# Kernel optimization log

Hardware: AMD Instinct MI355X
Metric: run time of the kernel (lower is better)

Reference implementation:

```python
import jax, jax.numpy as jnp
import numpy as np

N_NODES = 100000
N_EDGES = 1250000
D = 64


def _sage_conv(x, src, dst, W_l, b_l, W_r, n_nodes):
    # message = x[src]; scatter-mean onto dst; then lin_l(mean) + lin_r(x)
    msg = x[src]                                               # [E, D]
    agg = jax.ops.segment_sum(msg, dst, num_segments=n_nodes)  # [N, D]
    cnt = jax.ops.segment_sum(jnp.ones((src.shape[0],), x.dtype), dst,
                              num_segments=n_nodes)            # [N]
    mean = agg / jnp.maximum(cnt, 1.0)[:, None]
    return mean @ W_l + b_l + x @ W_r


def setup_inputs() -> dict:
    key = jax.random.key(0)
    ks = jax.random.split(key, 8)
    s = 1.0 / np.sqrt(D)
    x = jax.random.normal(ks[0], (N_NODES, D), dtype=jnp.float32)
    edge_index = jax.random.randint(ks[1], (2, N_EDGES), 0, N_NODES, dtype=jnp.int32)
    W_l1 = jax.random.normal(ks[2], (D, D), dtype=jnp.float32) * s
    b_l1 = jnp.zeros((D,), jnp.float32)
    W_r1 = jax.random.normal(ks[3], (D, D), dtype=jnp.float32) * s
    W_l2 = jax.random.normal(ks[4], (D, D), dtype=jnp.float32) * s
    b_l2 = jnp.zeros((D,), jnp.float32)
    W_r2 = jax.random.normal(ks[5], (D, D), dtype=jnp.float32) * s
    return {"x": x, "edge_index": edge_index,
            "W_l1": W_l1, "b_l1": b_l1, "W_r1": W_r1,
            "W_l2": W_l2, "b_l2": b_l2, "W_r2": W_r2}


def reference(x, edge_index, W_l1, b_l1, W_r1, W_l2, b_l2, W_r2):
    src, dst = edge_index[0], edge_index[1]
    n = x.shape[0]
    h = jax.nn.relu(_sage_conv(x, src, dst, W_l1, b_l1, W_r1, n))
    return _sage_conv(h, src, dst, W_l2, b_l2, W_r2, n)
```

## Files before the change

### kernel.cpp

```cpp
#include <hip/hip_runtime.h>

#define N_NODES 100000
#define N_EDGES 1250000
#define D 64
#define ZERO_NODE N_NODES

#define BIN_SHIFT 8
#define BIN_NODES 256
#define NBINS ((N_NODES + BIN_NODES - 1) >> BIN_SHIFT)
#define BIN_CAP 3712
#define BIN_SLAB (BIN_CAP + 3 * BIN_NODES)
#define CHUNK 2048
#define NCHUNK ((N_EDGES + CHUNK - 1) / CHUNK)
#define CCAP 32
#define CONV4 (N_NODES * D / 4)

#define SLAB_INTS (NBINS * BIN_SLAB)

typedef __attribute__((ext_vector_type(8))) short short8;
typedef __attribute__((ext_vector_type(4))) float f32x4;

__device__ inline unsigned short f2bf(float f) {
    unsigned int u = __float_as_uint(f);
    unsigned int r = (u + 0x7fffu + ((u >> 16) & 1u)) >> 16;
    return (unsigned short)r;
}
__device__ inline void acc_bf4(float4& c, uint2 u) {
    c.x += __uint_as_float(u.x << 16);
    c.y += __uint_as_float(u.x & 0xffff0000u);
    c.z += __uint_as_float(u.y << 16);
    c.w += __uint_as_float(u.y & 0xffff0000u);
}

__global__ __launch_bounds__(1024)
void part_convert_kernel(const float4* __restrict__ xin, ushort4* __restrict__ xb,
                         unsigned int* __restrict__ xb_zrow,
                         unsigned int* __restrict__ h_zrow,
                         const float* __restrict__ Wl1, const float* __restrict__ Wr1,
                         const float* __restrict__ Wl2, const float* __restrict__ Wr2,
                         unsigned short* __restrict__ wt,
                         const int* __restrict__ src, const int* __restrict__ dst,
                         int* __restrict__ cslab, unsigned short* __restrict__ ccnt) {
    __shared__ int lcur[NBINS];

    const int t = threadIdx.x;
    const int c = blockIdx.x;
    if (t < NBINS) lcur[t] = 0;

    const int g0 = c * 1024 + t;
    const int gsz = NCHUNK * 1024;
    for (int g = g0; g < CONV4; g += gsz) {
        float4 v = xin[g];
        ushort4 u;
        u.x = f2bf(v.x); u.y = f2bf(v.y); u.z = f2bf(v.z); u.w = f2bf(v.w);
        xb[g] = u;
    }
    if (g0 < 32) { xb_zrow[g0] = 0u; h_zrow[g0] = 0u; }
    if (g0 < 2 * 64 * 128) {
        int layer = g0 >> 13;
        int n = (g0 >> 7) & 63;
        int k = g0 & 127;
        const float* W = layer ? (k < 64 ? Wl2 : Wr2) : (k < 64 ? Wl1 : Wr1);
        wt[g0] = f2bf(W[(k & 63) * D + n]);
    }
    __syncthreads();

    const int e0 = c * CHUNK;
    int cnt = N_EDGES - e0; if (cnt > CHUNK) cnt = CHUNK;
    for (int i = t; i < cnt; i += 1024) {
        int d = dst[e0 + i];
        int s = src[e0 + i];
        int b = d >> BIN_SHIFT;
        int r = atomicAdd(&lcur[b], 1);
        if (r < CCAP)
            cslab[(c * NBINS + b) * CCAP + r] = (s << BIN_SHIFT) | (d & (BIN_NODES - 1));
    }
    __syncthreads();

    if (t < NBINS) {
        int v = lcur[t];
        ccnt[t * NCHUNK + c] = (unsigned short)(v < CCAP ? v : CCAP);
    }
}

__global__ __launch_bounds__(1024)
void build_kernel(const int* __restrict__ cslab, const unsigned short* __restrict__ ccnt,
                  int* __restrict__ deg_out, int* __restrict__ rstart_out,
                  int* __restrict__ slabs) {
    __shared__ int soff[NCHUNK];
    __shared__ int scnt[NCHUNK];
    __shared__ int stage[BIN_CAP];
    __shared__ int hist[BIN_NODES];
    __shared__ int cur[BIN_NODES];
    __shared__ int wsum[16];
    __shared__ int wsum2[16];
    __shared__ int tot_s;

    const int b = blockIdx.x;
    const int t = threadIdx.x;
    const int lane = t & 63, wave = t >> 6;
    const int nb0 = b << BIN_SHIFT;

    int v = (t < NCHUNK) ? (int)ccnt[b * NCHUNK + t] : 0;
    int sv = v;
    for (int off = 1; off < 64; off <<= 1) {
        int u = __shfl_up(sv, off);
        if (lane >= off) sv += u;
    }
    if (lane == 63) wsum[wave] = sv;
    if (t < BIN_NODES) hist[t] = 0;
    __syncthreads();
    int wpre = 0;
    for (int w = 0; w < wave; ++w) wpre += wsum[w];
    int excl = sv + wpre - v;
    if (t < NCHUNK) { soff[t] = excl; scnt[t] = v; }
    if (t == NCHUNK - 1) tot_s = excl + v;
    __syncthreads();

    int cntb = tot_s; if (cntb > BIN_CAP) cntb = BIN_CAP;

    if (t < NCHUNK) {
        int base = soff[t], n = scnt[t];
        const int* p = &cslab[(t * NBINS + b) * CCAP];
        for (int r = 0; r < n; ++r) {
            int pos = base + r;
            if (pos < BIN_CAP) stage[pos] = p[r];
        }
    }
    __syncthreads();

    for (int i = t; i < cntb; i += 1024)
        atomicAdd(&hist[stage[i] & (BIN_NODES - 1)], 1);
    __syncthreads();

    int h = (t < BIN_NODES) ? hist[t] : 0;
    int p = (h + 3) & ~3;
    int s2 = p;
    for (int off = 1; off < 64; off <<= 1) {
        int u = __shfl_up(s2, off);
        if (lane >= off) s2 += u;
    }
    if (lane == 63) wsum2[wave] = s2;
    __syncthreads();
    int wpre2 = 0;
    for (int w = 0; w < wave; ++w) wpre2 += wsum2[w];
    if (t < BIN_NODES) {
        int excl2 = s2 + wpre2 - p;
        int rs = b * BIN_SLAB + excl2;
        cur[t] = rs;
        int n = nb0 + t;
        if (n < N_NODES) {
            deg_out[n] = h;
            rstart_out[n] = rs;
            for (int j = h; j < p; ++j) slabs[rs + j] = ZERO_NODE;
        }
    }
    __syncthreads();

    for (int i = t; i < cntb; i += 1024) {
        int pk = stage[i];
        int pos = atomicAdd(&cur[pk & (BIN_NODES - 1)], 1);
        slabs[pos] = pk >> BIN_SHIFT;
    }
}

template <typename TOUT>
__global__ __launch_bounds__(256, 6)
void fused_layer_kernel(const unsigned short* __restrict__ xin,
                        const int* __restrict__ rstart,
                        const int* __restrict__ deg,
                        const int* __restrict__ sorted_src,
                        const unsigned short* __restrict__ wt,
                        const float* __restrict__ bl,
                        TOUT* __restrict__ out,
                        int relu) {
    __shared__ __align__(16) unsigned short sA[32][136];

    const uint2* __restrict__ xin64 = (const uint2*)xin;

    const int tid = threadIdx.x;
    const int row0 = blockIdx.x * 32;

    const int wave = tid >> 6;
    const int lane = tid & 63;
    const int q  = lane >> 4;
    const int f2 = lane & 15;

#pragma unroll
    for (int j = 0; j < 2; ++j) {
        const int rb = wave * 8 + 4 * j;
        const int n0 = row0 + rb, n1 = n0 + 1, n2 = n0 + 2, n3 = n0 + 3;

        int dg0 = deg[n0], dg1 = deg[n1], dg2 = deg[n2], dg3 = deg[n3];
        int st0 = rstart[n0], st1 = rstart[n1], st2 = rstart[n2], st3 = rstart[n3];
        int pd0 = (dg0 + 3) & ~3, pd1 = (dg1 + 3) & ~3;
        int pd2 = (dg2 + 3) & ~3, pd3 = (dg3 + 3) & ~3;
        int m0 = pd0 > 64 ? 64 : pd0, m1 = pd1 > 64 ? 64 : pd1;
        int m2 = pd2 > 64 ? 64 : pd2, m3 = pd3 > 64 ? 64 : pd3;

        int idx0 = ZERO_NODE, idx1 = ZERO_NODE, idx2 = ZERO_NODE, idx3 = ZERO_NODE;
        if (lane < m0) idx0 = sorted_src[st0 + lane];
        if (lane < m1) idx1 = sorted_src[st1 + lane];
        if (lane < m2) idx2 = sorted_src[st2 + lane];
        if (lane < m3) idx3 = sorted_src[st3 + lane];
        uint2 xr0 = xin64[(size_t)n0 * 16 + f2];
        uint2 xr1 = xin64[(size_t)n1 * 16 + f2];
        uint2 xr2 = xin64[(size_t)n2 * 16 + f2];
        uint2 xr3 = xin64[(size_t)n3 * 16 + f2];

        float4 c0 = make_float4(0.f, 0.f, 0.f, 0.f);
        float4 c1 = make_float4(0.f, 0.f, 0.f, 0.f);
        float4 c2 = make_float4(0.f, 0.f, 0.f, 0.f);
        float4 c3 = make_float4(0.f, 0.f, 0.f, 0.f);

        int q0 = m0 >> 2, q1 = m1 >> 2, q2 = m2 >> 2, q3 = m3 >> 2;
        int qa = q0 > q1 ? q0 : q1, qb = q2 > q3 ? q2 : q3;
        int quads = qa > qb ? qa : qb;
        int t = 0;
        for (; t + 2 <= quads; t += 2) {
            int e00 = __shfl(idx0, 4 * t + q), e01 = __shfl(idx0, 4 * t + 4 + q);
            int e10 = __shfl(idx1, 4 * t + q), e11 = __shfl(idx1, 4 * t + 4 + q);
            int e20 = __shfl(idx2, 4 * t + q), e21 = __shfl(idx2, 4 * t + 4 + q);
            int e30 = __shfl(idx3, 4 * t + q), e31 = __shfl(idx3, 4 * t + 4 + q);
            uint2 u00 = xin64[(size_t)e00 * 16 + f2];
            uint2 u01 = xin64[(size_t)e01 * 16 + f2];
            uint2 u10 = xin64[(size_t)e10 * 16 + f2];
            uint2 u11 = xin64[(size_t)e11 * 16 + f2];
            uint2 u20 = xin64[(size_t)e20 * 16 + f2];
            uint2 u21 = xin64[(size_t)e21 * 16 + f2];
            uint2 u30 = xin64[(size_t)e30 * 16 + f2];
            uint2 u31 = xin64[(size_t)e31 * 16 + f2];
            acc_bf4(c0, u00); acc_bf4(c0, u01);
            acc_bf4(c1, u10); acc_bf4(c1, u11);
            acc_bf4(c2, u20); acc_bf4(c2, u21);
            acc_bf4(c3, u30); acc_bf4(c3, u31);
        }
        for (; t < quads; ++t) {
            int e00 = __shfl(idx0, 4 * t + q);
            int e10 = __shfl(idx1, 4 * t + q);
            int e20 = __shfl(idx2, 4 * t + q);
            int e30 = __shfl(idx3, 4 * t + q);
            uint2 u00 = xin64[(size_t)e00 * 16 + f2];
            uint2 u10 = xin64[(size_t)e10 * 16 + f2];
            uint2 u20 = xin64[(size_t)e20 * 16 + f2];
            uint2 u30 = xin64[(size_t)e30 * 16 + f2];
            acc_bf4(c0, u00); acc_bf4(c1, u10);
            acc_bf4(c2, u20); acc_bf4(c3, u30);
        }

        if (__builtin_expect(pd0 > 64, 0)) {
            for (int base = 64; base < pd0; base += 64) {
                int m = pd0 - base; if (m > 64) m = 64;
                int idx = ZERO_NODE;
                if (lane < m) idx = sorted_src[st0 + base + lane];
                int qds = m >> 2;
                for (int tt = 0; tt < qds; ++tt) {
                    int e = __shfl(idx, 4 * tt + q);
                    acc_bf4(c0, xin64[(size_t)e * 16 + f2]);
                }
            }
        }
        if (__builtin_expect(pd1 > 64, 0)) {
            for (int base = 64; base < pd1; base += 64) {
                int m = pd1 - base; if (m > 64) m = 64;
                int idx = ZERO_NODE;
                if (lane < m) idx = sorted_src[st1 + base + lane];
                int qds = m >> 2;
                for (int tt = 0; tt < qds; ++tt) {
                    int e = __shfl(idx, 4 * tt + q);
                    acc_bf4(c1, xin64[(size_t)e * 16 + f2]);
                }
            }
        }
        if (__builtin_expect(pd2 > 64, 0)) {
            for (int base = 64; base < pd2; base += 64) {
                int m = pd2 - base; if (m > 64) m = 64;
                int idx = ZERO_NODE;
                if (lane < m) idx = sorted_src[st2 + base + lane];
                int qds = m >> 2;
                for (int tt = 0; tt < qds; ++tt) {
                    int e = __shfl(idx, 4 * tt + q);
                    acc_bf4(c2, xin64[(size_t)e * 16 + f2]);
                }
            }
        }
        if (__builtin_expect(pd3 > 64, 0)) {
            for (int base = 64; base < pd3; base += 64) {
                int m = pd3 - base; if (m > 64) m = 64;
                int idx = ZERO_NODE;
                if (lane < m) idx = sorted_src[st3 + base + lane];
                int qds = m >> 2;
                for (int tt = 0; tt < qds; ++tt) {
                    int e = __shfl(idx, 4 * tt + q);
                    acc_bf4(c3, xin64[(size_t)e * 16 + f2]);
                }
            }
        }

        c0.x += __shfl_xor(c0.x, 16); c0.y += __shfl_xor(c0.y, 16);
        c0.z += __shfl_xor(c0.z, 16); c0.w += __shfl_xor(c0.w, 16);
        c1.x += __shfl_xor(c1.x, 16); c1.y += __shfl_xor(c1.y, 16);
        c1.z += __shfl_xor(c1.z, 16); c1.w += __shfl_xor(c1.w, 16);
        c2.x += __shfl_xor(c2.x, 16); c2.y += __shfl_xor(c2.y, 16);
        c2.z += __shfl_xor(c2.z, 16); c2.w += __shfl_xor(c2.w, 16);
        c3.x += __shfl_xor(c3.x, 16); c3.y += __shfl_xor(c3.y, 16);
        c3.z += __shfl_xor(c3.z, 16); c3.w += __shfl_xor(c3.w, 16);
        c0.x += __shfl_xor(c0.x, 32); c0.y += __shfl_xor(c0.y, 32);
        c0.z += __shfl_xor(c0.z, 32); c0.w += __shfl_xor(c0.w, 32);
        c1.x += __shfl_xor(c1.x, 32); c1.y += __shfl_xor(c1.y, 32);
        c1.z += __shfl_xor(c1.z, 32); c1.w += __shfl_xor(c1.w, 32);
        c2.x += __shfl_xor(c2.x, 32); c2.y += __shfl_xor(c2.y, 32);
        c2.z += __shfl_xor(c2.z, 32); c2.w += __shfl_xor(c2.w, 32);
        c3.x += __shfl_xor(c3.x, 32); c3.y += __shfl_xor(c3.y, 32);
        c3.z += __shfl_xor(c3.z, 32); c3.w += __shfl_xor(c3.w, 32);

        float i0 = 1.0f / (float)(dg0 > 0 ? dg0 : 1);
        float i1 = 1.0f / (float)(dg1 > 0 ? dg1 : 1);
        float i2 = 1.0f / (float)(dg2 > 0 ? dg2 : 1);
        float i3 = 1.0f / (float)(dg3 > 0 ? dg3 : 1);
        if (q == 0) {
            unsigned int p0, p1;
            p0 = (unsigned int)f2bf(c0.x * i0) | ((unsigned int)f2bf(c0.y * i0) << 16);
            p1 = (unsigned int)f2bf(c0.z * i0) | ((unsigned int)f2bf(c0.w * i0) << 16);
            *(uint2*)&sA[rb + 0][f2 * 4] = make_uint2(p0, p1);
            *(uint2*)&sA[rb + 0][64 + f2 * 4] = xr0;
            p0 = (unsigned int)f2bf(c1.x * i1) | ((unsigned int)f2bf(c1.y * i1) << 16);
            p1 = (unsigned int)f2bf(c1.z * i1) | ((unsigned int)f2bf(c1.w * i1) << 16);
            *(uint2*)&sA[rb + 1][f2 * 4] = make_uint2(p0, p1);
            *(uint2*)&sA[rb + 1][64 + f2 * 4] = xr1;
            p0 = (unsigned int)f2bf(c2.x * i2) | ((unsigned int)f2bf(c2.y * i2) << 16);
            p1 = (unsigned int)f2bf(c2.z * i2) | ((unsigned int)f2bf(c2.w * i2) << 16);
            *(uint2*)&sA[rb + 2][f2 * 4] = make_uint2(p0, p1);
            *(uint2*)&sA[rb + 2][64 + f2 * 4] = xr2;
            p0 = (unsigned int)f2bf(c3.x * i3) | ((unsigned int)f2bf(c3.y * i3) << 16);
            p1 = (unsigned int)f2bf(c3.z * i3) | ((unsigned int)f2bf(c3.w * i3) << 16);
            *(uint2*)&sA[rb + 3][f2 * 4] = make_uint2(p0, p1);
            *(uint2*)&sA[rb + 3][64 + f2 * 4] = xr3;
        }
    }
    __syncthreads();

    const int tm = wave & 1;
    const int tn0 = (wave >> 1) * 2;
    const int mrow = tm * 16 + (lane & 15);
    const int kq = (lane >> 4) * 8;

    short8 afr[4];
#pragma unroll
    for (int kk = 0; kk < 4; ++kk)
        afr[kk] = *(const short8*)&sA[mrow][kk * 32 + kq];

#pragma unroll
    for (int ti = 0; ti < 2; ++ti) {
        const int tn = tn0 + ti;
        const int col = tn * 16 + (lane & 15);
        float bias = bl[col];
        f32x4 acc = {bias, bias, bias, bias};
#pragma unroll
        for (int kk = 0; kk < 4; ++kk) {
            short8 bfr = *(const short8*)&wt[col * 128 + kk * 32 + kq];
            acc = __builtin_amdgcn_mfma_f32_16x16x32_bf16(afr[kk], bfr, acc, 0, 0, 0);
        }
        const int r0 = row0 + tm * 16 + (lane >> 4) * 4;
#pragma unroll
        for (int reg = 0; reg < 4; ++reg) {
            float o = relu ? fmaxf(acc[reg], 0.f) : acc[reg];
            if constexpr (__hip_internal::is_same<TOUT, unsigned short>::value)
                out[(size_t)(r0 + reg) * D + col] = f2bf(o);
            else
                out[(size_t)(r0 + reg) * D + col] = o;
        }
    }
}

extern "C" void kernel_launch(void* const* d_in, const int* in_sizes, int n_in,
                              void* d_out, int out_size, void* d_ws, size_t ws_size,
                              hipStream_t stream) {
    const float* x   = (const float*)d_in[0];
    const int*   ei  = (const int*)d_in[1];
    const float* Wl1 = (const float*)d_in[2];
    const float* b1  = (const float*)d_in[3];
    const float* Wr1 = (const float*)d_in[4];
    const float* Wl2 = (const float*)d_in[5];
    const float* b2  = (const float*)d_in[6];
    const float* Wr2 = (const float*)d_in[7];

    const int* src = ei;
    const int* dst = ei + N_EDGES;

    int* cslab = (int*)d_ws;
    unsigned short* ccnt = (unsigned short*)(cslab + NCHUNK * NBINS * CCAP);
    int* deg    = cslab + NCHUNK * NBINS * CCAP + 120000;
    int* rstart = deg + N_NODES;
    int* slabs  = rstart + N_NODES;
    unsigned short* wt_all = (unsigned short*)(slabs + SLAB_INTS);
    unsigned short* wt1 = wt_all;
    unsigned short* wt2 = wt_all + 64 * 128;
    unsigned short* h = wt_all + 2 * 64 * 128;
    float* out = (float*)d_out;
    unsigned short* xb = (unsigned short*)d_out;

    const int dense_blocks = N_NODES / 32;

    part_convert_kernel<<<NCHUNK, 1024, 0, stream>>>(
        (const float4*)x, (ushort4*)xb,
        (unsigned int*)(xb + (size_t)ZERO_NODE * D),
        (unsigned int*)(h + (size_t)ZERO_NODE * D),
        Wl1, Wr1, Wl2, Wr2, wt_all,
        src, dst, cslab, ccnt);

    build_kernel<<<NBINS, 1024, 0, stream>>>(cslab, ccnt, deg, rstart, slabs);

    fused_layer_kernel<unsigned short><<<dense_blocks, 256, 0, stream>>>(
        xb, rstart, deg, slabs, wt1, b1, h, 1);
    fused_layer_kernel<float><<<dense_blocks, 256, 0, stream>>>(
        h, rstart, deg, slabs, wt2, b2, out, 0);
}
```

Baseline: 201.8 us.

## Fold CSR build into layer kernels with per-block LDS edge bucketing

Removes the separate build kernel. The partition kernel now bins edges into 32-node bins per 4096-edge chunk, and each fused layer block gathers its bin's chunk lists into shared memory. There it histograms and scatters them to form its own padded neighbour lists before aggregation. This drops one launch and the global slab round-trip. In exchange, the bucketing work is repeated in both layers, every block reads a small count array and slab covering all chunks, and fixed caps (16 per chunk-bin, 704 per bin) can silently drop edges if exceeded.

```diff
diff --git a/kernel.cpp b/kernel.cpp
--- a/kernel.cpp
+++ b/kernel.cpp
@@ -5,17 +5,16 @@
 #define D 64
 #define ZERO_NODE N_NODES
 
-#define BIN_SHIFT 8
-#define BIN_NODES 256
-#define NBINS ((N_NODES + BIN_NODES - 1) >> BIN_SHIFT)
-#define BIN_CAP 3712
-#define BIN_SLAB (BIN_CAP + 3 * BIN_NODES)
-#define CHUNK 2048
-#define NCHUNK ((N_EDGES + CHUNK - 1) / CHUNK)
-#define CCAP 32
+#define BSHIFT 5
+#define BINSZ 32
+#define NBIN (N_NODES / BINSZ)
+#define CH 4096
+#define NC ((N_EDGES + CH - 1) / CH)
+#define CAP 16
 #define CONV4 (N_NODES * D / 4)
 
-#define SLAB_INTS (NBINS * BIN_SLAB)
+#define RAWCAP 704
+#define ELCAP 832
 
 typedef __attribute__((ext_vector_type(8))) short short8;
 typedef __attribute__((ext_vector_type(4))) float f32x4;
@@ -40,15 +39,15 @@
                          const float* __restrict__ Wl2, const float* __restrict__ Wr2,
                          unsigned short* __restrict__ wt,
                          const int* __restrict__ src, const int* __restrict__ dst,
-                         int* __restrict__ cslab, unsigned short* __restrict__ ccnt) {
-    __shared__ int lcur[NBINS];
+                         int* __restrict__ cslab, unsigned char* __restrict__ ccnt) {
+    __shared__ int lcur[NBIN];
 
     const int t = threadIdx.x;
     const int c = blockIdx.x;
-    if (t < NBINS) lcur[t] = 0;
+    for (int i = t; i < NBIN; i += 1024) lcur[i] = 0;
 
     const int g0 = c * 1024 + t;
-    const int gsz = NCHUNK * 1024;
+    const int gsz = NC * 1024;
     for (int g = g0; g < CONV4; g += gsz) {
         float4 v = xin[g];
         ushort4 u;
@@ -65,148 +64,123 @@
     }
     __syncthreads();
 
-    const int e0 = c * CHUNK;
-    int cnt = N_EDGES - e0; if (cnt > CHUNK) cnt = CHUNK;
+    const int e0 = c * CH;
+    int cnt = N_EDGES - e0; if (cnt > CH) cnt = CH;
     for (int i = t; i < cnt; i += 1024) {
         int d = dst[e0 + i];
         int s = src[e0 + i];
-        int b = d >> BIN_SHIFT;
+        int b = d >> BSHIFT;
         int r = atomicAdd(&lcur[b], 1);
-        if (r < CCAP)
-            cslab[(c * NBINS + b) * CCAP + r] = (s << BIN_SHIFT) | (d & (BIN_NODES - 1));
-    }
-    __syncthreads();
-
-    if (t < NBINS) {
-        int v = lcur[t];
-        ccnt[t * NCHUNK + c] = (unsigned short)(v < CCAP ? v : CCAP);
-    }
-}
-
-__global__ __launch_bounds__(1024)
-void build_kernel(const int* __restrict__ cslab, const unsigned short* __restrict__ ccnt,
-                  int* __restrict__ deg_out, int* __restrict__ rstart_out,
-                  int* __restrict__ slabs) {
-    __shared__ int soff[NCHUNK];
-    __shared__ int scnt[NCHUNK];
-    __shared__ int stage[BIN_CAP];
-    __shared__ int hist[BIN_NODES];
-    __shared__ int cur[BIN_NODES];
-    __shared__ int wsum[16];
-    __shared__ int wsum2[16];
-    __shared__ int tot_s;
-
-    const int b = blockIdx.x;
-    const int t = threadIdx.x;
-    const int lane = t & 63, wave = t >> 6;
-    const int nb0 = b << BIN_SHIFT;
-
-    int v = (t < NCHUNK) ? (int)ccnt[b * NCHUNK + t] : 0;
-    int sv = v;
-    for (int off = 1; off < 64; off <<= 1) {
-        int u = __shfl_up(sv, off);
-        if (lane >= off) sv += u;
-    }
-    if (lane == 63) wsum[wave] = sv;
-    if (t < BIN_NODES) hist[t] = 0;
-    __syncthreads();
-    int wpre = 0;
-    for (int w = 0; w < wave; ++w) wpre += wsum[w];
-    int excl = sv + wpre - v;
-    if (t < NCHUNK) { soff[t] = excl; scnt[t] = v; }
-    if (t == NCHUNK - 1) tot_s = excl + v;
-    __syncthreads();
-
-    int cntb = tot_s; if (cntb > BIN_CAP) cntb = BIN_CAP;
-
-    if (t < NCHUNK) {
-        int base = soff[t], n = scnt[t];
-        const int* p = &cslab[(t * NBINS + b) * CCAP];
-        for (int r = 0; r < n; ++r) {
-            int pos = base + r;
-            if (pos < BIN_CAP) stage[pos] = p[r];
-        }
-    }
-    __syncthreads();
-
-    for (int i = t; i < cntb; i += 1024)
-        atomicAdd(&hist[stage[i] & (BIN_NODES - 1)], 1);
-    __syncthreads();
-
-    int h = (t < BIN_NODES) ? hist[t] : 0;
-    int p = (h + 3) & ~3;
-    int s2 = p;
-    for (int off = 1; off < 64; off <<= 1) {
-        int u = __shfl_up(s2, off);
-        if (lane >= off) s2 += u;
-    }
-    if (lane == 63) wsum2[wave] = s2;
-    __syncthreads();
-    int wpre2 = 0;
-    for (int w = 0; w < wave; ++w) wpre2 += wsum2[w];
-    if (t < BIN_NODES) {
-        int excl2 = s2 + wpre2 - p;
-        int rs = b * BIN_SLAB + excl2;
-        cur[t] = rs;
-        int n = nb0 + t;
-        if (n < N_NODES) {
-            deg_out[n] = h;
-            rstart_out[n] = rs;
-            for (int j = h; j < p; ++j) slabs[rs + j] = ZERO_NODE;
-        }
-    }
-    __syncthreads();
-
-    for (int i = t; i < cntb; i += 1024) {
-        int pk = stage[i];
-        int pos = atomicAdd(&cur[pk & (BIN_NODES - 1)], 1);
-        slabs[pos] = pk >> BIN_SHIFT;
+        if (r < CAP)
+            cslab[((size_t)b * NC + c) * CAP + r] = (s << BSHIFT) | (d & (BINSZ - 1));
+    }
+    __syncthreads();
+
+    for (int i = t; i < NBIN; i += 1024) {
+        int v = lcur[i];
+        ccnt[(size_t)i * NC + c] = (unsigned char)(v < CAP ? v : CAP);
     }
 }
 
 template <typename TOUT>
 __global__ __launch_bounds__(256, 6)
 void fused_layer_kernel(const unsigned short* __restrict__ xin,
-                        const int* __restrict__ rstart,
-                        const int* __restrict__ deg,
-                        const int* __restrict__ sorted_src,
+                        const int* __restrict__ cslab,
+                        const unsigned char* __restrict__ ccnt,
                         const unsigned short* __restrict__ wt,
                         const float* __restrict__ bl,
                         TOUT* __restrict__ out,
                         int relu) {
     __shared__ __align__(16) unsigned short sA[32][136];
+    __shared__ int raw[RAWCAP];
+    __shared__ int elist[ELCAP];
+    __shared__ int ehist[BINSZ];
+    __shared__ int ecur[BINSZ];
+    __shared__ int eoff[BINSZ];
+    __shared__ int edeg[BINSZ];
+    __shared__ unsigned char ccs[NC + 2];
+    __shared__ int etot;
 
     const uint2* __restrict__ xin64 = (const uint2*)xin;
 
     const int tid = threadIdx.x;
-    const int row0 = blockIdx.x * 32;
+    const int b = blockIdx.x;
+    const int row0 = b * BINSZ;
 
     const int wave = tid >> 6;
     const int lane = tid & 63;
     const int q  = lane >> 4;
     const int f2 = lane & 15;
 
+    if (tid < BINSZ) ehist[tid] = 0;
+    if (tid == 0) etot = 0;
+    for (int i = tid; i < NC; i += 256) ccs[i] = ccnt[(size_t)b * NC + i];
+    __syncthreads();
+
+    const int4* __restrict__ cb4 = (const int4*)(cslab + (size_t)b * NC * CAP);
+    for (int i = tid; i < NC * CAP / 4; i += 256) {
+        int c = i >> 2;
+        int rbase = (i & 3) * 4;
+        int vc = (int)ccs[c];
+        if (rbase < vc) {
+            int4 v4 = cb4[i];
+            int nv = vc - rbase; if (nv > 4) nv = 4;
+            int p = atomicAdd(&etot, nv);
+            if (p + nv <= RAWCAP) {
+                raw[p] = v4.x;                 atomicAdd(&ehist[v4.x & 31], 1);
+                if (nv > 1) { raw[p+1] = v4.y; atomicAdd(&ehist[v4.y & 31], 1); }
+                if (nv > 2) { raw[p+2] = v4.z; atomicAdd(&ehist[v4.z & 31], 1); }
+                if (nv > 3) { raw[p+3] = v4.w; atomicAdd(&ehist[v4.w & 31], 1); }
+            }
+        }
+    }
+    __syncthreads();
+
+    if (tid < BINSZ) {
+        int h = ehist[tid];
+        int p = (h + 3) & ~3;
+        int v = p;
+        for (int off = 1; off < 32; off <<= 1) {
+            int u = __shfl_up(v, off);
+            if (tid >= off) v += u;
+        }
+        int excl = v - p;
+        eoff[tid] = excl;
+        ecur[tid] = excl;
+        edeg[tid] = h;
+        for (int j = h; j < p; ++j) elist[excl + j] = ZERO_NODE;
+    }
+    __syncthreads();
+
+    int etc = etot; if (etc > RAWCAP) etc = RAWCAP;
+    for (int i = tid; i < etc; i += 256) {
+        int v = raw[i];
+        int p = atomicAdd(&ecur[v & 31], 1);
+        elist[p] = v >> BSHIFT;
+    }
+    __syncthreads();
+
 #pragma unroll
     for (int j = 0; j < 2; ++j) {
         const int rb = wave * 8 + 4 * j;
-        const int n0 = row0 + rb, n1 = n0 + 1, n2 = n0 + 2, n3 = n0 + 3;
-
-        int dg0 = deg[n0], dg1 = deg[n1], dg2 = deg[n2], dg3 = deg[n3];
-        int st0 = rstart[n0], st1 = rstart[n1], st2 = rstart[n2], st3 = rstart[n3];
+        int dg0 = edeg[rb + 0], dg1 = edeg[rb + 1];
+        int dg2 = edeg[rb + 2], dg3 = edeg[rb + 3];
+        int st0 = eoff[rb + 0], st1 = eoff[rb + 1];
+        int st2 = eoff[rb + 2], st3 = eoff[rb + 3];
         int pd0 = (dg0 + 3) & ~3, pd1 = (dg1 + 3) & ~3;
         int pd2 = (dg2 + 3) & ~3, pd3 = (dg3 + 3) & ~3;
         int m0 = pd0 > 64 ? 64 : pd0, m1 = pd1 > 64 ? 64 : pd1;
         int m2 = pd2 > 64 ? 64 : pd2, m3 = pd3 > 64 ? 64 : pd3;
 
         int idx0 = ZERO_NODE, idx1 = ZERO_NODE, idx2 = ZERO_NODE, idx3 = ZERO_NODE;
-        if (lane < m0) idx0 = sorted_src[st0 + lane];
-        if (lane < m1) idx1 = sorted_src[st1 + lane];
-        if (lane < m2) idx2 = sorted_src[st2 + lane];
-        if (lane < m3) idx3 = sorted_src[st3 + lane];
-        uint2 xr0 = xin64[(size_t)n0 * 16 + f2];
-        uint2 xr1 = xin64[(size_t)n1 * 16 + f2];
-        uint2 xr2 = xin64[(size_t)n2 * 16 + f2];
-        uint2 xr3 = xin64[(size_t)n3 * 16 + f2];
+        if (lane < m0) idx0 = elist[st0 + lane];
+        if (lane < m1) idx1 = elist[st1 + lane];
+        if (lane < m2) idx2 = elist[st2 + lane];
+        if (lane < m3) idx3 = elist[st3 + lane];
+        uint2 xr0 = xin64[(size_t)(row0 + rb + 0) * 16 + f2];
+        uint2 xr1 = xin64[(size_t)(row0 + rb + 1) * 16 + f2];
+        uint2 xr2 = xin64[(size_t)(row0 + rb + 2) * 16 + f2];
+        uint2 xr3 = xin64[(size_t)(row0 + rb + 3) * 16 + f2];
 
         float4 c0 = make_float4(0.f, 0.f, 0.f, 0.f);
         float4 c1 = make_float4(0.f, 0.f, 0.f, 0.f);
@@ -252,7 +226,7 @@
             for (int base = 64; base < pd0; base += 64) {
                 int m = pd0 - base; if (m > 64) m = 64;
                 int idx = ZERO_NODE;
-                if (lane < m) idx = sorted_src[st0 + base + lane];
+                if (lane < m) idx = elist[st0 + base + lane];
                 int qds = m >> 2;
                 for (int tt = 0; tt < qds; ++tt) {
                     int e = __shfl(idx, 4 * tt + q);
@@ -264,7 +238,7 @@
             for (int base = 64; base < pd1; base += 64) {
                 int m = pd1 - base; if (m > 64) m = 64;
                 int idx = ZERO_NODE;
-                if (lane < m) idx = sorted_src[st1 + base + lane];
+                if (lane < m) idx = elist[st1 + base + lane];
                 int qds = m >> 2;
                 for (int tt = 0; tt < qds; ++tt) {
                     int e = __shfl(idx, 4 * tt + q);
@@ -276,7 +250,7 @@
             for (int base = 64; base < pd2; base += 64) {
                 int m = pd2 - base; if (m > 64) m = 64;
                 int idx = ZERO_NODE;
-                if (lane < m) idx = sorted_src[st2 + base + lane];
+                if (lane < m) idx = elist[st2 + base + lane];
                 int qds = m >> 2;
                 for (int tt = 0; tt < qds; ++tt) {
                     int e = __shfl(idx, 4 * tt + q);
@@ -288,7 +262,7 @@
             for (int base = 64; base < pd3; base += 64) {
                 int m = pd3 - base; if (m > 64) m = 64;
                 int idx = ZERO_NODE;
-                if (lane < m) idx = sorted_src[st3 + base + lane];
+                if (lane < m) idx = elist[st3 + base + lane];
                 int qds = m >> 2;
                 for (int tt = 0; tt < qds; ++tt) {
                     int e = __shfl(idx, 4 * tt + q);
@@ -389,30 +363,24 @@
     const int* dst = ei + N_EDGES;
 
     int* cslab = (int*)d_ws;
-    unsigned short* ccnt = (unsigned short*)(cslab + NCHUNK * NBINS * CCAP);
-    int* deg    = cslab + NCHUNK * NBINS * CCAP + 120000;
-    int* rstart = deg + N_NODES;
-    int* slabs  = rstart + N_NODES;
-    unsigned short* wt_all = (unsigned short*)(slabs + SLAB_INTS);
+    unsigned char* ccnt = (unsigned char*)(cslab + (size_t)NBIN * NC * CAP);
+    size_t ccnt_bytes = ((size_t)NBIN * NC + 3) & ~(size_t)3;
+    unsigned short* wt_all = (unsigned short*)(ccnt + ccnt_bytes);
     unsigned short* wt1 = wt_all;
     unsigned short* wt2 = wt_all + 64 * 128;
     unsigned short* h = wt_all + 2 * 64 * 128;
     float* out = (float*)d_out;
     unsigned short* xb = (unsigned short*)d_out;
 
-    const int dense_blocks = N_NODES / 32;
-
-    part_convert_kernel<<<NCHUNK, 1024, 0, stream>>>(
+    part_convert_kernel<<<NC, 1024, 0, stream>>>(
         (const float4*)x, (ushort4*)xb,
         (unsigned int*)(xb + (size_t)ZERO_NODE * D),
         (unsigned int*)(h + (size_t)ZERO_NODE * D),
         Wl1, Wr1, Wl2, Wr2, wt_all,
         src, dst, cslab, ccnt);
 
-    build_kernel<<<NBINS, 1024, 0, stream>>>(cslab, ccnt, deg, rstart, slabs);
-
-    fused_layer_kernel<unsigned short><<<dense_blocks, 256, 0, stream>>>(
-        xb, rstart, deg, slabs, wt1, b1, h, 1);
-    fused_layer_kernel<float><<<dense_blocks, 256, 0, stream>>>(
-        h, rstart, deg, slabs, wt2, b2, out, 0);
-}
+    fused_layer_kernel<unsigned short><<<NBIN, 256, 0, stream>>>(
+        xb, cslab, ccnt, wt1, b1, h, 1);
+    fused_layer_kernel<float><<<NBIN, 256, 0, stream>>>(
+        h, cslab, ccnt, wt2, b2, out, 0);
+}
```

Result: slower. 227.2 us (+12.6%).
